# Performance work log

Measured on AMD Instinct MI355X. Metric: run time of the kernel, lower is better.

## Reference

```python
import jax, jax.numpy as jnp
import numpy as np

K = 3            # kernel_size
PAD = (K - 1) // 2
UM = 2           # um_dim
C_IN = 128
C_OUT = 128
SLOPE = 0.01     # F.leaky_relu default negative slope


def setup_inputs() -> dict:
    key = jax.random.key(0)
    k1, k2, k3 = jax.random.split(key, 3)
    xx = jax.random.normal(k1, (16, C_IN, 64, 64), dtype=jnp.float32)
    # Conv2d(C_in, C_out, K, stride=K, bias=True) parameters
    w = jax.random.normal(k2, (C_OUT, C_IN, K, K), dtype=jnp.float32) * 0.05
    b = jax.random.normal(k3, (C_OUT,), dtype=jnp.float32) * 0.05
    return {"xx": xx, "w": w, "b": b}


def reference(xx, w, b):
    B, C, H, Wd = xx.shape
    # --- unfold: replicate pad, then extract all KxK patches (stride 1) ---
    xp = jnp.pad(xx, ((0, 0), (0, 0), (PAD, PAD), (PAD, PAD)), mode="edge")
    # patches[b, c, r, s, i, j] = xp[b, c, i + r, j + s]   -> [B, C, K, K, H, W]
    patches = jnp.stack(
        [jnp.stack([xp[:, :, r:r + H, s:s + Wd] for s in range(K)], axis=2)
         for r in range(K)], axis=2)
    # --- subtract per-(um-slot, pixel) mean over channel groups and KxK ---
    g = patches.reshape(B, C // UM, UM, K, K, H, Wd)
    avgs = g.mean(axis=(1, 3, 4), keepdims=True)        # [B,1,UM,1,1,H,W]
    g = g - avgs
    p = g.reshape(B, C, K, K, H, Wd)
    # --- patch-wise conv (kernel_size == stride on the tiled image). The
    # torch code's transpose(2,4).transpose(-1,-2) tiling places patch col
    # offset s along tiled rows and row offset r along tiled cols, so the
    # conv weight w[o,c,r,s] pairs with patches[b,c,s,r,i,j]. ---
    out = jnp.einsum("ocrs,bcsrij->boij", w, p) + b[None, :, None, None]
    # leaky_relu
    out = jnp.where(out > 0, out, SLOPE * out)
    # --- add mean back per um-slot ---
    m = avgs[:, :, :, 0, 0]                             # [B,1,UM,H,W]
    O = out.shape[1]
    out = out.reshape(B, O // UM, UM, H, Wd) + m
    return out.reshape(B, O, H, Wd)
```

## Files before the change

kernel.cpp:

```cpp
#include <hip/hip_runtime.h>
#include <hip/hip_bf16.h>

typedef __bf16 bf16x8 __attribute__((ext_vector_type(8)));
typedef float  f32x4  __attribute__((ext_vector_type(4)));

#define NB 16
#define CI 128
#define CO 128
#define HH 64
#define WW 64

#define SROWS 4
#define SCOLS 66
#define SSTR  72

__global__ void prep(const float* __restrict__ w, __bf16* __restrict__ Ag,
                     float* __restrict__ wsum) {
    __shared__ float red[8];
    const int blk = blockIdx.x, tid = threadIdx.x;
    if (blk < 72) {
        int gid  = blk * 256 + tid;
        int l    = gid & 63;
        int frag = gid >> 6;
        int mt   = frag & 7;
        int t    = frag >> 3;
        int tap  = t >> 2;
        int r    = tap % 3;
        int s    = tap / 3;
        int o    = mt * 16 + (l & 15);
        int cb   = (t & 3) * 32 + (l >> 4) * 8;
        bf16x8 v;
        #pragma unroll
        for (int j = 0; j < 8; ++j)
            v[j] = (__bf16)w[((o * CI + cb + j) * 3 + r) * 3 + s];
        *(bf16x8*)(Ag + (size_t)gid * 8) = v;
    } else {
        int o = blk - 72;
        const float* p = w + (size_t)o * CI * 9;
        float se = 0.f, so = 0.f;
        for (int idx = tid; idx < CI * 9; idx += 256) {
            int c = idx / 9;
            float v = p[idx];
            if (c & 1) so += v; else se += v;
        }
        #pragma unroll
        for (int off = 32; off; off >>= 1) {
            se += __shfl_down(se, off);
            so += __shfl_down(so, off);
        }
        int wave = tid >> 6, lane = tid & 63;
        if (lane == 0) { red[wave * 2] = se; red[wave * 2 + 1] = so; }
        __syncthreads();
        if (tid == 0) {
            wsum[o]      = red[0] + red[2] + red[4] + red[6];
            wsum[CO + o] = red[1] + red[3] + red[5] + red[7];
        }
    }
}

__global__ __launch_bounds__(512, 4) void conv_main(
        const float* __restrict__ x,
        const float* __restrict__ bias,
        const float* __restrict__ wsum,
        const __bf16* __restrict__ Ag,
        float* __restrict__ out)
{
    __shared__ __align__(16) __bf16 slab[SROWS * SCOLS * SSTR];
    __shared__ float Srow[SROWS * SCOLS * 2];
    __shared__ float avgl[2 * 64 * 2];

    const int tid  = threadIdx.x;
    const int b    = blockIdx.y;
    const int row0 = blockIdx.x * 2;

    const float* xb = x + (size_t)b * CI * HH * WW;

    const int wave = tid >> 6, lane = tid & 63;
    const int wm = wave >> 1, wn = wave & 1;
    const int m = lane & 15, q = lane >> 4;

    f32x4 acc[2][4];
    #pragma unroll
    for (int i = 0; i < 2; ++i)
        #pragma unroll
        for (int j = 0; j < 4; ++j)
            acc[i][j] = (f32x4){0.f, 0.f, 0.f, 0.f};

    int bbase[4];
    #pragma unroll
    for (int nt = 0; nt < 4; ++nt)
        bbase[nt] = (wn * SCOLS + nt * 16 + m) * SSTR + q * 8;

    const __bf16* Aw = Ag + (size_t)(wm * 2) * 512 + (size_t)lane * 8;

    for (int half = 0; half < 2; ++half) {
        if (half) __syncthreads();
        for (int u = tid; u < SROWS * SCOLS * 8; u += 512) {
            int col = u % SCOLS;
            int rc  = u / SCOLS;
            int cg  = rc & 7;
            int r   = rc >> 3;
            int yi  = row0 - 1 + r; yi = yi < 0 ? 0 : (yi > HH - 1 ? HH - 1 : yi);
            int xi  = col - 1;      xi = xi < 0 ? 0 : (xi > WW - 1 ? WW - 1 : xi);
            const float* src = xb + (size_t)(half * 64 + cg * 8) * (HH * WW)
                                  + yi * WW + xi;
            bf16x8 v;
            #pragma unroll
            for (int j = 0; j < 8; ++j)
                v[j] = (__bf16)src[(size_t)j * (HH * WW)];
            *(bf16x8*)(slab + (r * SCOLS + col) * SSTR + cg * 8) = v;
        }
        __syncthreads();
        for (int u = tid; u < SROWS * SCOLS; u += 512) {
            const __bf16* p = slab + u * SSTR;
            float se = 0.f, so = 0.f;
            #pragma unroll
            for (int cg = 0; cg < 8; ++cg) {
                bf16x8 v = *(const bf16x8*)(p + cg * 8);
                se += (float)v[0] + (float)v[2] + (float)v[4] + (float)v[6];
                so += (float)v[1] + (float)v[3] + (float)v[5] + (float)v[7];
            }
            if (half) { se += Srow[u * 2 + 0]; so += Srow[u * 2 + 1]; }
            Srow[u * 2 + 0] = se;
            Srow[u * 2 + 1] = so;
        }
        __syncthreads();
        if (half == 1) {
            if (tid < 256) {
                int uu  = tid & 1;
                int col = (tid >> 1) & 63;
                int rr  = tid >> 7;
                float ssum = 0.f;
                #pragma unroll
                for (int dy = 0; dy < 3; ++dy)
                    #pragma unroll
                    for (int dx = 0; dx < 3; ++dx)
                        ssum += Srow[(((rr + dy) * SCOLS) + (col + dx)) * 2 + uu];
                avgl[tid] = ssum * (1.0f / 576.0f);
            }
            __syncthreads();
        }
        #pragma unroll
        for (int tap = 0; tap < 9; ++tap) {
            const int s_ = tap / 3, r3 = tap % 3;
            const int boff0 = (s_ * SCOLS + r3) * SSTR;
            #pragma unroll
            for (int cc = 0; cc < 2; ++cc) {
                const int t    = tap * 4 + half * 2 + cc;
                const int boff = boff0 + cc * 32;
                bf16x8 bfrag[4];
                #pragma unroll
                for (int nt = 0; nt < 4; ++nt)
                    bfrag[nt] = *(const bf16x8*)(slab + bbase[nt] + boff);
                bf16x8 afrag[2];
                #pragma unroll
                for (int i = 0; i < 2; ++i)
                    afrag[i] = *(const bf16x8*)(Aw + (size_t)t * 4096 + i * 512);
                #pragma unroll
                for (int i = 0; i < 2; ++i)
                    #pragma unroll
                    for (int nt = 0; nt < 4; ++nt)
                        acc[i][nt] = __builtin_amdgcn_mfma_f32_16x16x32_bf16(
                            afrag[i], bfrag[nt], acc[i][nt], 0, 0, 0);
            }
        }
    }

    float a0v[4], a1v[4];
    #pragma unroll
    for (int nt = 0; nt < 4; ++nt) {
        int col = nt * 16 + m;
        a0v[nt] = avgl[(wn * 64 + col) * 2 + 0];
        a1v[nt] = avgl[(wn * 64 + col) * 2 + 1];
    }
    float* outb = out + (size_t)b * CO * HH * WW + (size_t)(row0 + wn) * WW;
    #pragma unroll
    for (int i = 0; i < 2; ++i) {
        #pragma unroll
        for (int rg = 0; rg < 4; ++rg) {
            int o = wm * 32 + i * 16 + q * 4 + rg;
            float bo = bias[o];
            float w0 = wsum[o];
            float w1 = wsum[CO + o];
            float* po = outb + (size_t)o * (HH * WW);
            #pragma unroll
            for (int nt = 0; nt < 4; ++nt) {
                float v = acc[i][nt][rg] + bo - a0v[nt] * w0 - a1v[nt] * w1;
                v = v > 0.f ? v : 0.01f * v;
                v += (o & 1) ? a1v[nt] : a0v[nt];
                po[nt * 16 + m] = v;
            }
        }
    }
}

extern "C" void kernel_launch(void* const* d_in, const int* in_sizes, int n_in,
                              void* d_out, int out_size, void* d_ws, size_t ws_size,
                              hipStream_t stream) {
    const float* x    = (const float*)d_in[0];
    const float* w    = (const float*)d_in[1];
    const float* bias = (const float*)d_in[2];
    float* out = (float*)d_out;

    __bf16* Ag   = (__bf16*)d_ws;
    float*  wsum = (float*)((char*)d_ws + 294912);

    prep<<<200, 256, 0, stream>>>(w, Ag, wsum);

    dim3 grid(HH / 2, NB);
    conv_main<<<grid, 512, 0, stream>>>(x, bias, wsum, Ag, out);
}
```

Baseline: 104.6 us.

## Remap wave tiling to 4x2 MFMA tiles with prefetched A fragments

Changes the per-wave output tile from 2 M-tiles by 4 N-tiles to 4 M-tiles by 2 N-tiles, splitting pixels across rows and half-columns so each wave covers 64 output channels. The weight (A) fragments from global memory are software-prefetched one iteration ahead in a rolled 18-step loop, hiding global load latency behind MFMAs. Output stores become nontemporal. Trade-off: more A-fragment global traffic per wave and more registers for the double-buffered A fragments, but fewer LDS B reads.

```diff
diff --git a/kernel.cpp b/kernel.cpp
--- a/kernel.cpp
+++ b/kernel.cpp
@@ -76,24 +76,32 @@
     const float* xb = x + (size_t)b * CI * HH * WW;
 
     const int wave = tid >> 6, lane = tid & 63;
-    const int wm = wave >> 1, wn = wave & 1;
+    const int wm = wave >> 2;
+    const int wn = wave & 3;
+    const int rsel = wn >> 1, csel = wn & 1;
     const int m = lane & 15, q = lane >> 4;
 
-    f32x4 acc[2][4];
-    #pragma unroll
-    for (int i = 0; i < 2; ++i)
-        #pragma unroll
-        for (int j = 0; j < 4; ++j)
+    f32x4 acc[4][2];
+    #pragma unroll
+    for (int i = 0; i < 4; ++i)
+        #pragma unroll
+        for (int j = 0; j < 2; ++j)
             acc[i][j] = (f32x4){0.f, 0.f, 0.f, 0.f};
 
-    int bbase[4];
-    #pragma unroll
-    for (int nt = 0; nt < 4; ++nt)
-        bbase[nt] = (wn * SCOLS + nt * 16 + m) * SSTR + q * 8;
-
-    const __bf16* Aw = Ag + (size_t)(wm * 2) * 512 + (size_t)lane * 8;
+    int bbase[2];
+    #pragma unroll
+    for (int nt = 0; nt < 2; ++nt)
+        bbase[nt] = (rsel * SCOLS + csel * 32 + nt * 16 + m) * SSTR + q * 8;
+
+    const __bf16* Abase = Ag + ((size_t)(wm * 4) << 9) + ((size_t)lane << 3);
 
     for (int half = 0; half < 2; ++half) {
+        const int t0 = half * 2;
+        bf16x8 Acur[4];
+        #pragma unroll
+        for (int i = 0; i < 4; ++i)
+            Acur[i] = *(const bf16x8*)(Abase + (t0 << 12) + (i << 9));
+
         if (half) __syncthreads();
         for (int u = tid; u < SROWS * SCOLS * 8; u += 512) {
             int col = u % SCOLS;
@@ -140,55 +148,57 @@
             }
             __syncthreads();
         }
-        #pragma unroll
-        for (int tap = 0; tap < 9; ++tap) {
-            const int s_ = tap / 3, r3 = tap % 3;
-            const int boff0 = (s_ * SCOLS + r3) * SSTR;
-            #pragma unroll
-            for (int cc = 0; cc < 2; ++cc) {
-                const int t    = tap * 4 + half * 2 + cc;
-                const int boff = boff0 + cc * 32;
-                bf16x8 bfrag[4];
+        for (int it = 0; it < 18; ++it) {
+            int itn  = it + 1 < 18 ? it + 1 : it;
+            int tn   = (itn >> 1) * 4 + half * 2 + (itn & 1);
+            bf16x8 Anx[4];
+            #pragma unroll
+            for (int i = 0; i < 4; ++i)
+                Anx[i] = *(const bf16x8*)(Abase + (tn << 12) + (i << 9));
+            int tap = it >> 1, cc = it & 1;
+            int s_  = tap >= 6 ? 2 : (tap >= 3 ? 1 : 0);
+            int r3  = tap - s_ * 3;
+            int boff = (s_ * SCOLS + r3) * SSTR + cc * 32;
+            bf16x8 Bf[2];
+            #pragma unroll
+            for (int nt = 0; nt < 2; ++nt)
+                Bf[nt] = *(const bf16x8*)(slab + bbase[nt] + boff);
+            #pragma unroll
+            for (int i = 0; i < 4; ++i)
                 #pragma unroll
-                for (int nt = 0; nt < 4; ++nt)
-                    bfrag[nt] = *(const bf16x8*)(slab + bbase[nt] + boff);
-                bf16x8 afrag[2];
-                #pragma unroll
-                for (int i = 0; i < 2; ++i)
-                    afrag[i] = *(const bf16x8*)(Aw + (size_t)t * 4096 + i * 512);
-                #pragma unroll
-                for (int i = 0; i < 2; ++i)
-                    #pragma unroll
-                    for (int nt = 0; nt < 4; ++nt)
-                        acc[i][nt] = __builtin_amdgcn_mfma_f32_16x16x32_bf16(
-                            afrag[i], bfrag[nt], acc[i][nt], 0, 0, 0);
-            }
-        }
-    }
-
-    float a0v[4], a1v[4];
-    #pragma unroll
-    for (int nt = 0; nt < 4; ++nt) {
-        int col = nt * 16 + m;
-        a0v[nt] = avgl[(wn * 64 + col) * 2 + 0];
-        a1v[nt] = avgl[(wn * 64 + col) * 2 + 1];
-    }
-    float* outb = out + (size_t)b * CO * HH * WW + (size_t)(row0 + wn) * WW;
-    #pragma unroll
-    for (int i = 0; i < 2; ++i) {
+                for (int nt = 0; nt < 2; ++nt)
+                    acc[i][nt] = __builtin_amdgcn_mfma_f32_16x16x32_bf16(
+                        Acur[i], Bf[nt], acc[i][nt], 0, 0, 0);
+            #pragma unroll
+            for (int i = 0; i < 4; ++i)
+                Acur[i] = Anx[i];
+        }
+    }
+
+    float a0v[2], a1v[2];
+    #pragma unroll
+    for (int nt = 0; nt < 2; ++nt) {
+        int col = csel * 32 + nt * 16 + m;
+        a0v[nt] = avgl[rsel * 128 + col * 2 + 0];
+        a1v[nt] = avgl[rsel * 128 + col * 2 + 1];
+    }
+    float* outb = out + (size_t)b * CO * HH * WW + (size_t)(row0 + rsel) * WW
+                      + csel * 32;
+    #pragma unroll
+    for (int i = 0; i < 4; ++i) {
         #pragma unroll
         for (int rg = 0; rg < 4; ++rg) {
-            int o = wm * 32 + i * 16 + q * 4 + rg;
+            int o = wm * 64 + i * 16 + q * 4 + rg;
             float bo = bias[o];
             float w0 = wsum[o];
             float w1 = wsum[CO + o];
             float* po = outb + (size_t)o * (HH * WW);
             #pragma unroll
-            for (int nt = 0; nt < 4; ++nt) {
+            for (int nt = 0; nt < 2; ++nt) {
                 float v = acc[i][nt][rg] + bo - a0v[nt] * w0 - a1v[nt] * w1;
                 v = v > 0.f ? v : 0.01f * v;
                 v += (o & 1) ? a1v[nt] : a0v[nt];
-                po[nt * 16 + m] = v;
+                __builtin_nontemporal_store(v, po + nt * 16 + m);
             }
         }
     }
```

Result: slower. 112.7 us (+7.7%).
